# Kernel optimization log

Measured on AMD Instinct MI355X. Metric: run time of the kernel, lower is better.

Reference implementation:

```python
import jax, jax.numpy as jnp
import numpy as np

BN_EPS = 1e-3  # Keras BatchNormalization default epsilon

def _bn(x, p):
    # p: [4, d] = gamma, beta, moving_mean, moving_var (inference-mode BN)
    g, b, m, v = p[0], p[1], p[2], p[3]
    return g * (x - m) * jax.lax.rsqrt(v + BN_EPS) + b

def _ffn_block(x, pbn, w, c):
    # BatchNorm -> Dropout(identity at inference) -> Dense(gelu, exact erf like tf.nn.gelu)
    return jax.nn.gelu(_bn(x, pbn) @ w + c, approximate=False)

def setup_inputs() -> dict:
    key = jax.random.key(0)
    ks = jax.random.split(key, 16)
    N, E, D, H = 100000, 1600000, 64, 64
    def bn_pack(k, d):
        k1, k2, k3, k4 = jax.random.split(k, 4)
        gamma = 1.0 + 0.1 * jax.random.normal(k1, (d,), jnp.float32)
        beta = 0.1 * jax.random.normal(k2, (d,), jnp.float32)
        mean = 0.05 * jax.random.normal(k3, (d,), jnp.float32)
        var = jax.random.uniform(k4, (d,), jnp.float32, 0.5, 1.5)
        return jnp.stack([gamma, beta, mean, var], axis=0)
    def dense(k, fan_in, fan_out):
        return (jax.random.normal(k, (fan_in, fan_out), jnp.float32) / np.sqrt(fan_in)).astype(jnp.float32)
    return {
        "x": jax.random.normal(ks[0], (N, D), jnp.float32),
        "edges": jax.random.randint(ks[1], (2, E), 0, N, jnp.int32),
        "ew": jax.random.uniform(ks[2], (E,), jnp.float32),
        "pbn1": bn_pack(ks[3], D),
        "pw1": dense(ks[4], D, H),
        "pc1": 0.01 * jax.random.normal(ks[5], (H,), jnp.float32),
        "pbn2": bn_pack(ks[6], H),
        "pw2": dense(ks[7], H, H),
        "pc2": 0.01 * jax.random.normal(ks[8], (H,), jnp.float32),
        "ubn1": bn_pack(ks[9], D + H),
        "uw1": dense(ks[10], D + H, H),
        "uc1": 0.01 * jax.random.normal(ks[11], (H,), jnp.float32),
        "ubn2": bn_pack(ks[12], H),
        "uw2": dense(ks[13], H, H),
        "uc2": 0.01 * jax.random.normal(ks[14], (H,), jnp.float32),
    }

def reference(x, edges, ew, pbn1, pw1, pc1, pbn2, pw2, pc2, ubn1, uw1, uc1, ubn2, uw2, uc2):
    N = x.shape[0]
    node_idx, nbr_idx = edges[0], edges[1]
    # gather neighbour representations -> prepare FFN -> edge-weight scaling
    nbr = x[nbr_idx]                                   # [E, D]
    h = _ffn_block(nbr, pbn1, pw1, pc1)                # [E, H]
    h = _ffn_block(h, pbn2, pw2, pc2)                  # [E, H]
    msgs = h * ew[:, None]
    # unsorted_segment_mean: sum / count (0 for empty segments)
    s = jax.ops.segment_sum(msgs, node_idx, num_segments=N)            # [N, H]
    cnt = jax.ops.segment_sum(jnp.ones_like(ew), node_idx, num_segments=N)
    agg = s / jnp.maximum(cnt, 1.0)[:, None]
    # combination_type='concat' -> update FFN
    hcat = jnp.concatenate([x, agg], axis=1)           # [N, D+H]
    out = _ffn_block(hcat, ubn1, uw1, uc1)
    out = _ffn_block(out, ubn2, uw2, uc2)              # [N, H]
    return out
```

## Files before the change

### kernel.cpp

```cpp
#include <hip/hip_runtime.h>
#include <hip/hip_bf16.h>
#include <hip/hip_fp16.h>

#define BN_EPS 1e-3f
#define GSH 6
#define GNODES 64
#define NB_MAX 1600
#define BIN_E 4096
#define CAP_SH 11
#define BKT_CAP 2048

typedef __attribute__((ext_vector_type(8))) short short8;
typedef __attribute__((ext_vector_type(4))) float f32x4;

__device__ __forceinline__ float gelu_exact(float v) {
    return 0.5f * v * (1.0f + erff(v * 0.70710678118654752440f));
}
__device__ __forceinline__ short f2b(float f) {
    __hip_bfloat16 h = __float2bfloat16(f);
    return *reinterpret_cast<short*>(&h);
}

union Y16 { uint4 u; __half2 h[4]; };

struct MatDesc {
    const float* bn; const float* W; const float* c;
    short* Wswz; float* cp; int K; int base;
};

__global__ void __launch_bounds__(256) prep_all(
    const float* pbn1, const float* pw1, const float* pc1,
    const float* pbn2, const float* pw2, const float* pc2,
    const float* ubn1, const float* uw1, const float* uc1,
    const float* ubn2, const float* uw2, const float* uc2,
    short* W1s, float* c1p, short* W2s, float* c2p,
    short* U1s, float* uc1p, short* U2s, float* uc2p,
    int* __restrict__ gcur, int NB) {
    __shared__ float red[4][64];
    const MatDesc md[4] = {
        {pbn1, pw1, pc1, W1s, c1p, 64, 0},
        {pbn2, pw2, pc2, W2s, c2p, 64, 4096},
        {ubn1, uw1, uc1, U1s, uc1p, 128, 8192},
        {ubn2, uw2, uc2, U2s, uc2p, 64, 16384},
    };
    const int bid = blockIdx.x;
    if (bid < 20) {
        for (int gidx = bid * 256 + threadIdx.x; gidx < 20480; gidx += 20 * 256) {
            int m = (gidx < 4096) ? 0 : (gidx < 8192) ? 1 : (gidx < 16384) ? 2 : 3;
            const MatDesc& d = md[m];
            int idx = gidx - d.base;
            int KC = d.K / 32;
            int j = idx & 7, lane = (idx >> 3) & 63, f = idx >> 9;
            int h = f % KC, t = f / KC;
            int k = h * 32 + (lane >> 4) * 8 + j;
            int col = t * 16 + (lane & 15);
            float s = d.bn[k] * rsqrtf(d.bn[3 * d.K + k] + BN_EPS);
            d.Wswz[idx] = f2b(s * d.W[k * 64 + col]);
        }
    } else if (bid < 24) {
        const MatDesc& d = md[bid - 20];
        const int j = threadIdx.x & 63, kk = threadIdx.x >> 6;
        const int chunk = d.K / 4;
        float acc = 0.f;
        for (int i = 0; i < chunk; ++i) {
            int k = kk * chunk + i;
            float s = d.bn[k] * rsqrtf(d.bn[3 * d.K + k] + BN_EPS);
            float t = d.bn[d.K + k] - d.bn[2 * d.K + k] * s;
            acc += t * d.W[k * 64 + j];
        }
        red[kk][j] = acc;
        __syncthreads();
        if (threadIdx.x < 64)
            d.cp[j] = d.c[j] + red[0][j] + red[1][j] + red[2][j] + red[3][j];
    } else {
        int i = (bid - 24) * 256 + threadIdx.x;
        if (i < NB) gcur[i] = i << CAP_SH;
    }
}

__global__ void __launch_bounds__(256) ffn2_mfma(
    const float* __restrict__ X,
    const short* __restrict__ W1s, const float* __restrict__ c1,
    const short* __restrict__ W2s, const float* __restrict__ c2,
    __half* __restrict__ outv, int N) {
    __shared__ short Hs[4][16][72];
    const int tid = threadIdx.x;
    const int lane = tid & 63;
    const int wv = tid >> 6;
    const int lm = lane & 15, lh = lane >> 4;
    const int r0 = blockIdx.x * 64 + wv * 16;
    if (r0 >= N) return;
    const int rowA = min(r0 + lm, N - 1);

    short8 a[2];
    {
        const float* xp = X + (size_t)rowA * 64 + lh * 8;
#pragma unroll
        for (int h = 0; h < 2; ++h) {
            float4 u0 = *reinterpret_cast<const float4*>(xp + h * 32);
            float4 u1 = *reinterpret_cast<const float4*>(xp + h * 32 + 4);
            short8 r;
            r[0] = f2b(u0.x); r[1] = f2b(u0.y); r[2] = f2b(u0.z); r[3] = f2b(u0.w);
            r[4] = f2b(u1.x); r[5] = f2b(u1.y); r[6] = f2b(u1.z); r[7] = f2b(u1.w);
            a[h] = r;
        }
    }

#pragma unroll
    for (int t = 0; t < 4; ++t) {
        float cb = c1[t * 16 + lm];
        f32x4 acc = {cb, cb, cb, cb};
#pragma unroll
        for (int h = 0; h < 2; ++h) {
            short8 b = *reinterpret_cast<const short8*>(
                W1s + ((size_t)(t * 2 + h) * 64 + lane) * 8);
            acc = __builtin_amdgcn_mfma_f32_16x16x32_bf16(a[h], b, acc, 0, 0, 0);
        }
#pragma unroll
        for (int q = 0; q < 4; ++q)
            Hs[wv][4 * lh + q][t * 16 + lm] = f2b(gelu_exact(acc[q]));
    }

    short8 a2[2];
#pragma unroll
    for (int h = 0; h < 2; ++h)
        a2[h] = *reinterpret_cast<const short8*>(&Hs[wv][lm][h * 32 + lh * 8]);

#pragma unroll
    for (int t = 0; t < 4; ++t) {
        float cb = c2[t * 16 + lm];
        f32x4 acc = {cb, cb, cb, cb};
#pragma unroll
        for (int h = 0; h < 2; ++h) {
            short8 b = *reinterpret_cast<const short8*>(
                W2s + ((size_t)(t * 2 + h) * 64 + lane) * 8);
            acc = __builtin_amdgcn_mfma_f32_16x16x32_bf16(a2[h], b, acc, 0, 0, 0);
        }
#pragma unroll
        for (int q = 0; q < 4; ++q) {
            int row = r0 + 4 * lh + q;
            if (row < N)
                outv[(size_t)row * 64 + t * 16 + lm] = __float2half(gelu_exact(acc[q]));
        }
    }
}

__global__ void __launch_bounds__(256) bin_atomic(
    const int* __restrict__ node_idx, const int* __restrict__ nbr_idx,
    const float* __restrict__ ew, int* __restrict__ gcur,
    unsigned* __restrict__ es2, int E, int NB) {
    __shared__ int cntL[NB_MAX];
    const int tid = threadIdx.x;
    for (int i = tid; i < NB; i += 256) cntL[i] = 0;
    __syncthreads();
    const int base = blockIdx.x * BIN_E;
    const int end = min(base + BIN_E, E);
    for (int e = base + tid; e < end; e += 256)
        atomicAdd(&cntL[node_idx[e] >> GSH], 1);
    __syncthreads();
    for (int i = tid; i < NB; i += 256) {
        int c = cntL[i];
        if (c) cntL[i] = atomicAdd(&gcur[i], c);
    }
    __syncthreads();
    for (int e = base + tid; e < end; e += 512) {
        const int e1 = e + 256;
        int n0 = node_idx[e];
        unsigned q0 = (unsigned)(ew[e] * 511.f + 0.5f);
        unsigned p0 = ((unsigned)nbr_idx[e] << 15) | ((unsigned)(n0 & (GNODES - 1)) << 9) | q0;
        int n1 = 0; unsigned p1 = 0;
        const bool v1 = e1 < end;
        if (v1) {
            n1 = node_idx[e1];
            unsigned q1 = (unsigned)(ew[e1] * 511.f + 0.5f);
            p1 = ((unsigned)nbr_idx[e1] << 15) | ((unsigned)(n1 & (GNODES - 1)) << 9) | q1;
        }
        int s0 = atomicAdd(&cntL[n0 >> GSH], 1);
        int s1 = v1 ? atomicAdd(&cntL[n1 >> GSH], 1) : 0;
        if (s0 < ((n0 >> GSH) + 1) << CAP_SH) es2[s0] = p0;
        if (v1 && s1 < ((n1 >> GSH) + 1) << CAP_SH) es2[s1] = p1;
    }
}

__global__ void __launch_bounds__(256) agg_uffn(
    const __half* __restrict__ yh, const unsigned* __restrict__ es2,
    const int* __restrict__ gcur, const float* __restrict__ X,
    const short* __restrict__ U1s, const float* __restrict__ c1,
    const short* __restrict__ U2s, const float* __restrict__ c2,
    float* __restrict__ out, int N) {
    __shared__ unsigned pay[BKT_CAP];
    __shared__ short S[4][16][72];
    __shared__ int offL[GNODES + 1];
    __shared__ int curL[GNODES];
    const int tid = threadIdx.x;
    const int lane = tid & 63;
    const int wv = tid >> 6;
    const int b = blockIdx.x;
    const int s0 = b << CAP_SH;
    const int tot = min(gcur[b] - s0, BKT_CAP);

    unsigned ec[8];
    bool val[8];
#pragma unroll
    for (int c = 0; c < 8; ++c) {
        int i = tid + c * 256;
        val[c] = i < tot;
        ec[c] = val[c] ? es2[s0 + i] : 0u;
    }
    if (tid < GNODES) offL[tid] = 0;
    __syncthreads();
#pragma unroll
    for (int c = 0; c < 8; ++c)
        if (val[c]) atomicAdd(&offL[(ec[c] >> 9) & (GNODES - 1)], 1);
    __syncthreads();
    if (wv == 0) {
        int v = offL[lane], orig = v;
#pragma unroll
        for (int d = 1; d < 64; d <<= 1) {
            int n = __shfl_up(v, (unsigned)d, 64);
            if (lane >= d) v += n;
        }
        offL[lane] = v - orig;
        curL[lane] = v - orig;
        if (lane == 63) offL[64] = v;
    }
    __syncthreads();
#pragma unroll
    for (int c = 0; c < 8; ++c) {
        if (val[c]) {
            int slot = atomicAdd(&curL[(ec[c] >> 9) & (GNODES - 1)], 1);
            pay[slot] = ec[c];
        }
    }
    __syncthreads();

    const int g = lane >> 3, lg = lane & 7;
#pragma unroll
    for (int pass = 0; pass < 2; ++pass) {
        const int nn = pass * 8 + g;
        const int lo = offL[wv * 16 + nn], hi = offL[wv * 16 + nn + 1];
        __half2 acc2[4];
        const __half2 z = __float2half2_rn(0.f);
        acc2[0] = z; acc2[1] = z; acc2[2] = z; acc2[3] = z;
        int k = lo;
        for (; k + 1 < hi; k += 2) {
            unsigned e0 = pay[k], e1 = pay[k + 1];
            __half2 w0 = __half2half2(__float2half((float)(e0 & 511u) * (1.f / 511.f)));
            __half2 w1 = __half2half2(__float2half((float)(e1 & 511u) * (1.f / 511.f)));
            Y16 y0, y1;
            y0.u = *reinterpret_cast<const uint4*>(yh + (size_t)(e0 >> 15) * 64 + lg * 8);
            y1.u = *reinterpret_cast<const uint4*>(yh + (size_t)(e1 >> 15) * 64 + lg * 8);
#pragma unroll
            for (int j = 0; j < 4; ++j) acc2[j] = __hfma2(w0, y0.h[j], acc2[j]);
#pragma unroll
            for (int j = 0; j < 4; ++j) acc2[j] = __hfma2(w1, y1.h[j], acc2[j]);
        }
        if (k < hi) {
            unsigned e = pay[k];
            __half2 w = __half2half2(__float2half((float)(e & 511u) * (1.f / 511.f)));
            Y16 yv;
            yv.u = *reinterpret_cast<const uint4*>(yh + (size_t)(e >> 15) * 64 + lg * 8);
#pragma unroll
            for (int j = 0; j < 4; ++j) acc2[j] = __hfma2(w, yv.h[j], acc2[j]);
        }
        float rc = 1.f / fmaxf((float)(hi - lo), 1.f);
        short8 o;
#pragma unroll
        for (int j = 0; j < 4; ++j) {
            o[2 * j]     = f2b(__low2float(acc2[j]) * rc);
            o[2 * j + 1] = f2b(__high2float(acc2[j]) * rc);
        }
        *reinterpret_cast<short8*>(&S[wv][nn][lg * 8]) = o;
    }

    const int lm = lane & 15, lh = lane >> 4;
    const int r0 = b * 64 + wv * 16;
    if (r0 >= N) return;
    const int rowA = min(r0 + lm, N - 1);

    short8 a[4];
    {
        const float* xp = X + (size_t)rowA * 64 + lh * 8;
#pragma unroll
        for (int h = 0; h < 2; ++h) {
            float4 u0 = *reinterpret_cast<const float4*>(xp + h * 32);
            float4 u1 = *reinterpret_cast<const float4*>(xp + h * 32 + 4);
            short8 r;
            r[0] = f2b(u0.x); r[1] = f2b(u0.y); r[2] = f2b(u0.z); r[3] = f2b(u0.w);
            r[4] = f2b(u1.x); r[5] = f2b(u1.y); r[6] = f2b(u1.z); r[7] = f2b(u1.w);
            a[h] = r;
        }
#pragma unroll
        for (int h = 0; h < 2; ++h)
            a[2 + h] = *reinterpret_cast<const short8*>(&S[wv][lm][h * 32 + lh * 8]);
    }

#pragma unroll
    for (int t = 0; t < 4; ++t) {
        float cb = c1[t * 16 + lm];
        f32x4 acc = {cb, cb, cb, cb};
#pragma unroll
        for (int h = 0; h < 4; ++h) {
            short8 bb = *reinterpret_cast<const short8*>(
                U1s + ((size_t)(t * 4 + h) * 64 + lane) * 8);
            acc = __builtin_amdgcn_mfma_f32_16x16x32_bf16(a[h], bb, acc, 0, 0, 0);
        }
#pragma unroll
        for (int q = 0; q < 4; ++q)
            S[wv][4 * lh + q][t * 16 + lm] = f2b(gelu_exact(acc[q]));
    }

    short8 a2[2];
#pragma unroll
    for (int h = 0; h < 2; ++h)
        a2[h] = *reinterpret_cast<const short8*>(&S[wv][lm][h * 32 + lh * 8]);

#pragma unroll
    for (int t = 0; t < 4; ++t) {
        float cb = c2[t * 16 + lm];
        f32x4 acc = {cb, cb, cb, cb};
#pragma unroll
        for (int h = 0; h < 2; ++h) {
            short8 bb = *reinterpret_cast<const short8*>(
                U2s + ((size_t)(t * 2 + h) * 64 + lane) * 8);
            acc = __builtin_amdgcn_mfma_f32_16x16x32_bf16(a2[h], bb, acc, 0, 0, 0);
        }
#pragma unroll
        for (int q = 0; q < 4; ++q) {
            int row = r0 + 4 * lh + q;
            if (row < N)
                out[(size_t)row * 64 + t * 16 + lm] = gelu_exact(acc[q]);
        }
    }
}

extern "C" void kernel_launch(void* const* d_in, const int* in_sizes, int n_in,
                              void* d_out, int out_size, void* d_ws, size_t ws_size,
                              hipStream_t stream) {
    const float* x    = (const float*)d_in[0];
    const int*   edges= (const int*)d_in[1];
    const float* ew   = (const float*)d_in[2];
    const float* pbn1 = (const float*)d_in[3];
    const float* pw1  = (const float*)d_in[4];
    const float* pc1  = (const float*)d_in[5];
    const float* pbn2 = (const float*)d_in[6];
    const float* pw2  = (const float*)d_in[7];
    const float* pc2  = (const float*)d_in[8];
    const float* ubn1 = (const float*)d_in[9];
    const float* uw1  = (const float*)d_in[10];
    const float* uc1  = (const float*)d_in[11];
    const float* ubn2 = (const float*)d_in[12];
    const float* uw2  = (const float*)d_in[13];
    const float* uc2  = (const float*)d_in[14];
    float* out = (float*)d_out;

    const int N = in_sizes[0] / 64;
    const int E = in_sizes[2];
    const int* node_idx = edges;
    const int* nbr_idx  = edges + E;
    const int NB = (N + GNODES - 1) / GNODES;
    const int NBLK = (E + BIN_E - 1) / BIN_E;

    char* p = (char*)d_ws;
    auto alloc = [&](size_t bytes) {
        char* q = p;
        p += (bytes + 255) & ~(size_t)255;
        return q;
    };
    __half*   yh   = (__half*)alloc((size_t)N * 64 * 2);
    unsigned* es2  = (unsigned*)alloc((size_t)NB * BKT_CAP * 4);
    int*      gcur = (int*)alloc((size_t)NB * 4);
    short*    W1s  = (short*)alloc(4096 * 2);
    short*    W2s  = (short*)alloc(4096 * 2);
    short*    U1s  = (short*)alloc(8192 * 2);
    short*    U2s  = (short*)alloc(4096 * 2);
    float*    c1p  = (float*)alloc(64 * 4);
    float*    c2p  = (float*)alloc(64 * 4);
    float*    uc1p = (float*)alloc(64 * 4);
    float*    uc2p = (float*)alloc(64 * 4);

    prep_all<<<32, 256, 0, stream>>>(pbn1, pw1, pc1, pbn2, pw2, pc2,
                                     ubn1, uw1, uc1, ubn2, uw2, uc2,
                                     W1s, c1p, W2s, c2p, U1s, uc1p, U2s, uc2p,
                                     gcur, NB);
    bin_atomic<<<NBLK, 256, 0, stream>>>(node_idx, nbr_idx, ew, gcur, es2, E, NB);
    ffn2_mfma<<<(N + 63) / 64, 256, 0, stream>>>(x, W1s, c1p, W2s, c2p, yh, N);
    agg_uffn<<<NB, 256, 0, stream>>>(yh, es2, gcur, x, U1s, uc1p, U2s, uc2p, out, N);
}
```

Measured before the change: 111.4 us.

## Fuse edge binning with node FFN kernel and rework aggregation scatter

Merges the edge-binning kernel and the per-node prepare-FFN kernel into one launch, with the block index choosing the role, so the two independent phases run concurrently on the GPU. Binning blocks now handle twice as many edges each, and all loads are hoisted into registers before the shared-memory atomics. In agg_uffn, per-wave histograms replace the single shared counter array to reduce atomic contention. The neighbour gather processes two nodes at once with clamped indices so more loads are in flight, at the cost of wasted work when the two segment lengths differ. The larger register footprint in binning blocks may lower occupancy for the whole fused kernel.

```diff
diff --git a/kernel.cpp b/kernel.cpp
--- a/kernel.cpp
+++ b/kernel.cpp
@@ -6,7 +6,7 @@
 #define GSH 6
 #define GNODES 64
 #define NB_MAX 1600
-#define BIN_E 4096
+#define BIN_E 8192
 #define CAP_SH 11
 #define BKT_CAP 2048
 
@@ -78,17 +78,61 @@
     }
 }
 
-__global__ void __launch_bounds__(256) ffn2_mfma(
+__global__ void __launch_bounds__(256) bin_ffn2(
+    const int* __restrict__ node_idx, const int* __restrict__ nbr_idx,
+    const float* __restrict__ ew, int* __restrict__ gcur,
+    unsigned* __restrict__ es2,
     const float* __restrict__ X,
     const short* __restrict__ W1s, const float* __restrict__ c1,
     const short* __restrict__ W2s, const float* __restrict__ c2,
-    __half* __restrict__ outv, int N) {
+    __half* __restrict__ yh, int E, int NB, int NBLK, int N) {
+    __shared__ int cntL[NB_MAX];
     __shared__ short Hs[4][16][72];
     const int tid = threadIdx.x;
+
+    if (blockIdx.x < NBLK) {
+        for (int i = tid; i < NB; i += 256) cntL[i] = 0;
+        const int base = blockIdx.x * BIN_E;
+        const int end = min(base + BIN_E, E);
+        int nd[32];
+        unsigned pl[32];
+        bool vl[32];
+#pragma unroll
+        for (int j = 0; j < 32; ++j) {
+            int e = base + tid + j * 256;
+            vl[j] = e < end;
+            int ee = vl[j] ? e : base;
+            int n = node_idx[ee];
+            unsigned q = (unsigned)(ew[ee] * 511.f + 0.5f);
+            nd[j] = n;
+            pl[j] = ((unsigned)nbr_idx[ee] << 15) |
+                    ((unsigned)(n & (GNODES - 1)) << 9) | q;
+        }
+        __syncthreads();
+#pragma unroll
+        for (int j = 0; j < 32; ++j)
+            if (vl[j]) atomicAdd(&cntL[nd[j] >> GSH], 1);
+        __syncthreads();
+        for (int i = tid; i < NB; i += 256) {
+            int c = cntL[i];
+            if (c) cntL[i] = atomicAdd(&gcur[i], c);
+        }
+        __syncthreads();
+#pragma unroll
+        for (int j = 0; j < 32; ++j) {
+            if (vl[j]) {
+                int b = nd[j] >> GSH;
+                int s = atomicAdd(&cntL[b], 1);
+                if (s < ((b + 1) << CAP_SH)) es2[s] = pl[j];
+            }
+        }
+        return;
+    }
+
     const int lane = tid & 63;
     const int wv = tid >> 6;
     const int lm = lane & 15, lh = lane >> 4;
-    const int r0 = blockIdx.x * 64 + wv * 16;
+    const int r0 = (blockIdx.x - NBLK) * 64 + wv * 16;
     if (r0 >= N) return;
     const int rowA = min(r0 + lm, N - 1);
 
@@ -140,45 +184,8 @@
         for (int q = 0; q < 4; ++q) {
             int row = r0 + 4 * lh + q;
             if (row < N)
-                outv[(size_t)row * 64 + t * 16 + lm] = __float2half(gelu_exact(acc[q]));
-        }
-    }
-}
-
-__global__ void __launch_bounds__(256) bin_atomic(
-    const int* __restrict__ node_idx, const int* __restrict__ nbr_idx,
-    const float* __restrict__ ew, int* __restrict__ gcur,
-    unsigned* __restrict__ es2, int E, int NB) {
-    __shared__ int cntL[NB_MAX];
-    const int tid = threadIdx.x;
-    for (int i = tid; i < NB; i += 256) cntL[i] = 0;
-    __syncthreads();
-    const int base = blockIdx.x * BIN_E;
-    const int end = min(base + BIN_E, E);
-    for (int e = base + tid; e < end; e += 256)
-        atomicAdd(&cntL[node_idx[e] >> GSH], 1);
-    __syncthreads();
-    for (int i = tid; i < NB; i += 256) {
-        int c = cntL[i];
-        if (c) cntL[i] = atomicAdd(&gcur[i], c);
-    }
-    __syncthreads();
-    for (int e = base + tid; e < end; e += 512) {
-        const int e1 = e + 256;
-        int n0 = node_idx[e];
-        unsigned q0 = (unsigned)(ew[e] * 511.f + 0.5f);
-        unsigned p0 = ((unsigned)nbr_idx[e] << 15) | ((unsigned)(n0 & (GNODES - 1)) << 9) | q0;
-        int n1 = 0; unsigned p1 = 0;
-        const bool v1 = e1 < end;
-        if (v1) {
-            n1 = node_idx[e1];
-            unsigned q1 = (unsigned)(ew[e1] * 511.f + 0.5f);
-            p1 = ((unsigned)nbr_idx[e1] << 15) | ((unsigned)(n1 & (GNODES - 1)) << 9) | q1;
-        }
-        int s0 = atomicAdd(&cntL[n0 >> GSH], 1);
-        int s1 = v1 ? atomicAdd(&cntL[n1 >> GSH], 1) : 0;
-        if (s0 < ((n0 >> GSH) + 1) << CAP_SH) es2[s0] = p0;
-        if (v1 && s1 < ((n1 >> GSH) + 1) << CAP_SH) es2[s1] = p1;
+                yh[(size_t)row * 64 + t * 16 + lm] = __float2half(gelu_exact(acc[q]));
+        }
     }
 }
 
@@ -190,8 +197,9 @@
     float* __restrict__ out, int N) {
     __shared__ unsigned pay[BKT_CAP];
     __shared__ short S[4][16][72];
+    __shared__ int offW[4][GNODES];
+    __shared__ int curW[4][GNODES];
     __shared__ int offL[GNODES + 1];
-    __shared__ int curL[GNODES];
     const int tid = threadIdx.x;
     const int lane = tid & 63;
     const int wv = tid >> 6;
@@ -207,70 +215,91 @@
         val[c] = i < tot;
         ec[c] = val[c] ? es2[s0 + i] : 0u;
     }
-    if (tid < GNODES) offL[tid] = 0;
+    offW[wv][lane] = 0;
     __syncthreads();
 #pragma unroll
     for (int c = 0; c < 8; ++c)
-        if (val[c]) atomicAdd(&offL[(ec[c] >> 9) & (GNODES - 1)], 1);
+        if (val[c]) atomicAdd(&offW[wv][(ec[c] >> 9) & (GNODES - 1)], 1);
     __syncthreads();
     if (wv == 0) {
-        int v = offL[lane], orig = v;
+        int c0 = offW[0][lane], c1w = offW[1][lane];
+        int c2w = offW[2][lane], c3 = offW[3][lane];
+        int v = c0 + c1w + c2w + c3;
+        const int orig = v;
 #pragma unroll
         for (int d = 1; d < 64; d <<= 1) {
             int n = __shfl_up(v, (unsigned)d, 64);
             if (lane >= d) v += n;
         }
-        offL[lane] = v - orig;
-        curL[lane] = v - orig;
+        int ex = v - orig;
+        offL[lane] = ex;
         if (lane == 63) offL[64] = v;
+        curW[0][lane] = ex;
+        curW[1][lane] = ex + c0;
+        curW[2][lane] = ex + c0 + c1w;
+        curW[3][lane] = ex + c0 + c1w + c2w;
     }
     __syncthreads();
 #pragma unroll
     for (int c = 0; c < 8; ++c) {
         if (val[c]) {
-            int slot = atomicAdd(&curL[(ec[c] >> 9) & (GNODES - 1)], 1);
+            int slot = atomicAdd(&curW[wv][(ec[c] >> 9) & (GNODES - 1)], 1);
             pay[slot] = ec[c];
         }
     }
     __syncthreads();
 
     const int g = lane >> 3, lg = lane & 7;
-#pragma unroll
-    for (int pass = 0; pass < 2; ++pass) {
-        const int nn = pass * 8 + g;
-        const int lo = offL[wv * 16 + nn], hi = offL[wv * 16 + nn + 1];
-        __half2 acc2[4];
+    {
+        const int nA = wv * 16 + g, nB = nA + 8;
+        const int loA = offL[nA], hiA = offL[nA + 1];
+        const int loB = offL[nB], hiB = offL[nB + 1];
+        const int lenA = hiA - loA, lenB = hiB - loB;
+        const int kmax = max(lenA, lenB);
+        __half2 accA[4], accB[4];
         const __half2 z = __float2half2_rn(0.f);
-        acc2[0] = z; acc2[1] = z; acc2[2] = z; acc2[3] = z;
-        int k = lo;
-        for (; k + 1 < hi; k += 2) {
-            unsigned e0 = pay[k], e1 = pay[k + 1];
-            __half2 w0 = __half2half2(__float2half((float)(e0 & 511u) * (1.f / 511.f)));
-            __half2 w1 = __half2half2(__float2half((float)(e1 & 511u) * (1.f / 511.f)));
-            Y16 y0, y1;
-            y0.u = *reinterpret_cast<const uint4*>(yh + (size_t)(e0 >> 15) * 64 + lg * 8);
-            y1.u = *reinterpret_cast<const uint4*>(yh + (size_t)(e1 >> 15) * 64 + lg * 8);
-#pragma unroll
-            for (int j = 0; j < 4; ++j) acc2[j] = __hfma2(w0, y0.h[j], acc2[j]);
-#pragma unroll
-            for (int j = 0; j < 4; ++j) acc2[j] = __hfma2(w1, y1.h[j], acc2[j]);
-        }
-        if (k < hi) {
-            unsigned e = pay[k];
-            __half2 w = __half2half2(__float2half((float)(e & 511u) * (1.f / 511.f)));
-            Y16 yv;
-            yv.u = *reinterpret_cast<const uint4*>(yh + (size_t)(e >> 15) * 64 + lg * 8);
-#pragma unroll
-            for (int j = 0; j < 4; ++j) acc2[j] = __hfma2(w, yv.h[j], acc2[j]);
-        }
-        float rc = 1.f / fmaxf((float)(hi - lo), 1.f);
-        short8 o;
+#pragma unroll
+        for (int j = 0; j < 4; ++j) { accA[j] = z; accB[j] = z; }
+        for (int k = 0; k < kmax; k += 2) {
+#pragma unroll
+            for (int u = 0; u < 2; ++u) {
+                const int kk = k + u;
+                {
+                    const bool v = kk < lenA;
+                    unsigned e = pay[max(min(loA + kk, hiA - 1), 0)];
+                    float wf = v ? (float)(e & 511u) * (1.f / 511.f) : 0.f;
+                    __half2 w = __half2half2(__float2half(wf));
+                    Y16 y;
+                    y.u = *reinterpret_cast<const uint4*>(
+                        yh + (size_t)(e >> 15) * 64 + lg * 8);
+#pragma unroll
+                    for (int j = 0; j < 4; ++j) accA[j] = __hfma2(w, y.h[j], accA[j]);
+                }
+                {
+                    const bool v = kk < lenB;
+                    unsigned e = pay[max(min(loB + kk, hiB - 1), 0)];
+                    float wf = v ? (float)(e & 511u) * (1.f / 511.f) : 0.f;
+                    __half2 w = __half2half2(__float2half(wf));
+                    Y16 y;
+                    y.u = *reinterpret_cast<const uint4*>(
+                        yh + (size_t)(e >> 15) * 64 + lg * 8);
+#pragma unroll
+                    for (int j = 0; j < 4; ++j) accB[j] = __hfma2(w, y.h[j], accB[j]);
+                }
+            }
+        }
+        float rcA = 1.f / fmaxf((float)lenA, 1.f);
+        float rcB = 1.f / fmaxf((float)lenB, 1.f);
+        short8 oA, oB;
 #pragma unroll
         for (int j = 0; j < 4; ++j) {
-            o[2 * j]     = f2b(__low2float(acc2[j]) * rc);
-            o[2 * j + 1] = f2b(__high2float(acc2[j]) * rc);
-        }
-        *reinterpret_cast<short8*>(&S[wv][nn][lg * 8]) = o;
+            oA[2 * j]     = f2b(__low2float(accA[j]) * rcA);
+            oA[2 * j + 1] = f2b(__high2float(accA[j]) * rcA);
+            oB[2 * j]     = f2b(__low2float(accB[j]) * rcB);
+            oB[2 * j + 1] = f2b(__high2float(accB[j]) * rcB);
+        }
+        *reinterpret_cast<short8*>(&S[wv][g][lg * 8]) = oA;
+        *reinterpret_cast<short8*>(&S[wv][g + 8][lg * 8]) = oB;
     }
 
     const int lm = lane & 15, lh = lane >> 4;
@@ -360,6 +389,7 @@
     const int* nbr_idx  = edges + E;
     const int NB = (N + GNODES - 1) / GNODES;
     const int NBLK = (E + BIN_E - 1) / BIN_E;
+    const int FBLK = (N + 63) / 64;
 
     char* p = (char*)d_ws;
     auto alloc = [&](size_t bytes) {
@@ -383,7 +413,8 @@
                                      ubn1, uw1, uc1, ubn2, uw2, uc2,
                                      W1s, c1p, W2s, c2p, U1s, uc1p, U2s, uc2p,
                                      gcur, NB);
-    bin_atomic<<<NBLK, 256, 0, stream>>>(node_idx, nbr_idx, ew, gcur, es2, E, NB);
-    ffn2_mfma<<<(N + 63) / 64, 256, 0, stream>>>(x, W1s, c1p, W2s, c2p, yh, N);
+    bin_ffn2<<<NBLK + FBLK, 256, 0, stream>>>(node_idx, nbr_idx, ew, gcur, es2,
+                                              x, W1s, c1p, W2s, c2p, yh,
+                                              E, NB, NBLK, N);
     agg_uffn<<<NB, 256, 0, stream>>>(yh, es2, gcur, x, U1s, uc1p, U2s, uc2p, out, N);
 }
```

Result: faster. 96.08 us, median of 2 (-13.7%).
